# Performance work log

Measured on AMD Instinct MI355X. Metric: run time of the kernel, lower is better.

Reference implementation:

```python
import jax, jax.numpy as jnp
import numpy as np

B, S, DM, H = 4, 1024, 1024, 16
DK = DM // H  # 64, must equal embeddim=64

def _linear(x, W, b):
    # torch nn.Linear: y = x @ W.T + b, W is [out, in]
    return jnp.matmul(x, W.T) + b

def setup_inputs() -> dict:
    key = jax.random.key(0)
    ks = jax.random.split(key, 40)
    inp = {}
    inp["query"] = jax.random.normal(ks[0], (B, S, DM), jnp.float32)
    inp["key"] = jax.random.normal(ks[1], (B, S, DM), jnp.float32)
    inp["value"] = jax.random.normal(ks[2], (B, S, DM), jnp.float32)
    inp["mask"] = jnp.ones((B, S, S), jnp.int32)
    def mk(i, dout, din):
        W = jax.random.normal(ks[i], (dout, din), jnp.float32) / np.sqrt(din).astype(np.float32)
        b = jax.random.normal(ks[i + 20], (dout,), jnp.float32) * 0.01
        return W, b
    # the 4 d_model x d_model projection linears (q, k, v, out)
    inp["Wq"], inp["bq"] = mk(3, DM, DM)
    inp["Wk"], inp["bk"] = mk(4, DM, DM)
    inp["Wv"], inp["bv"] = mk(5, DM, DM)
    inp["Wo"], inp["bo"] = mk(6, DM, DM)
    # the 64x64 refinement linears
    inp["Wkl"], inp["bkl"] = mk(7, DK, DK)   # key_linear
    inp["Wql"], inp["bql"] = mk(8, DK, DK)   # query_linear
    inp["Wq2"], inp["bq2"] = mk(9, DK, DK)   # query2_linear
    inp["Wvl"], inp["bvl"] = mk(10, DK, DK)  # value_linear
    inp["Wel"], inp["bel"] = mk(11, DK, DK)  # embed_linear
    return inp

def reference(query, key, value, mask,
              Wq, bq, Wk, bk, Wv, bv, Wo, bo,
              Wkl, bkl, Wql, bql, Wq2, bq2, Wvl, bvl, Wel, bel):
    b, s, dm = query.shape
    # project and split heads: [b, h, s, d_k]
    def split(x):
        return x.reshape(b, s, H, DK).transpose(0, 2, 1, 3)
    q = split(_linear(query, Wq, bq))
    k = split(_linear(key, Wk, bk))
    v = split(_linear(value, Wv, bv))
    # per-head 64x64 refinements with relu
    key_refine = jax.nn.relu(_linear(k, Wkl, bkl))
    q1 = jax.nn.relu(_linear(q, Wql, bql))
    q1 = jax.nn.relu(_linear(q1, Wel, bel))
    q2 = jax.nn.relu(_linear(q, Wq2, bq2))
    v_refine = jax.nn.relu(_linear(v, Wvl, bvl))
    # two attention-like matmuls (no 1/sqrt(d_k) scaling in original)
    qv = jnp.einsum("bhqd,bhkd->bhqk", q2, v_refine)
    kq = jnp.einsum("bhqd,bhkd->bhqk", q1, key_refine)
    m = mask[:, None, :, :]  # mask.unsqueeze(1)
    kq = jnp.where(m == 0, jnp.float32(-1e9), kq)
    attn = jax.nn.softmax(kq, axis=-1)
    # elementwise combine, then matmul against raw projected key (not value!)
    out = jnp.einsum("bhqk,bhkd->bhqd", attn * qv, k)
    out = out.transpose(0, 2, 1, 3).reshape(b, s, dm)
    return _linear(out, Wo, bo)
```

## Files before the change

kernel.cpp:

```cpp
#include <hip/hip_runtime.h>
#include <hip/hip_bf16.h>

#define B_  4
#define S_  1024
#define DM_ 1024
#define H_  16
#define DK_ 64

typedef unsigned short u16;
typedef __attribute__((ext_vector_type(8))) short bf16x8;
typedef __attribute__((ext_vector_type(4))) float f32x4;

__device__ __forceinline__ float bf2f(u16 u) {
    union { unsigned int i; float f; } c;
    c.i = ((unsigned int)u) << 16;
    return c.f;
}
__device__ __forceinline__ u16 f2bf(float f) {
    union { float f; unsigned int i; } c;
    c.f = f;
    unsigned int x = c.i;
    unsigned int lsb = (x >> 16) & 1u;
    x += 0x7fffu + lsb;
    return (u16)(x >> 16);
}
__device__ __forceinline__ u16 f2bf_fast(float f) {
    __hip_bfloat16 h = __float2bfloat16(f);
    return *reinterpret_cast<u16*>(&h);
}

__device__ __forceinline__ void async_ld16(const u16* g, u16* l) {
    __builtin_amdgcn_global_load_lds(
        (const __attribute__((address_space(1))) unsigned int*)(const void*)g,
        (__attribute__((address_space(3))) unsigned int*)(void*)l, 16, 0, 0);
}

__global__ void detect_kernel(const u16* __restrict__ q, int* __restrict__ flag) {
    int lane = threadIdx.x & 63;
    int cnt = 0;
#pragma unroll
    for (int i = 0; i < 4; ++i) {
        u16 u = q[2 * (lane * 4 + i)];
        int e = (u >> 7) & 0xFF;
        cnt += (e >= 100 && e <= 140) ? 1 : 0;
    }
#pragma unroll
    for (int off = 1; off < 64; off <<= 1) cnt += __shfl_xor(cnt, off, 64);
    if (lane == 0) *flag = (cnt < 128) ? 1 : 0;
}

#define NSEG 12
struct CvtArgs {
    const void* src[NSEG];
    void*       dst[NSEG];
    unsigned    off[NSEG + 1];
};

__global__ __launch_bounds__(256) void prep_kernel(
    CvtArgs a, unsigned total, const int* __restrict__ flag,
    const int* __restrict__ mask, int* __restrict__ tflags)
{
    const int tid = threadIdx.x;
    if (blockIdx.x < 512) {
        const int bx = blockIdx.x;
        const int kt = bx & 15, b = (bx >> 4) & 3, z = bx >> 6;
        int ok = 1;
#pragma unroll
        for (int i = tid; i < 128 * 16; i += 256) {
            int row = z * 128 + (i >> 4), seg = i & 15;
            int4 m = *(const int4*)&mask[((size_t)b * S_ + row) * S_ + kt * 64 + seg * 4];
            ok &= (m.x != 0) & (m.y != 0) & (m.z != 0) & (m.w != 0);
        }
        if (!ok) atomicOr(&tflags[b * 16 + kt], 1);
        return;
    }
    if (!*flag) return;
    unsigned v = (blockIdx.x - 512) * 256 + tid;
    if (v >= total) return;
    int s = 0;
    while (s < NSEG - 1 && v >= a.off[s + 1]) ++s;
    unsigned local = v - a.off[s];
    u16* dp = (u16*)a.dst[s] + (size_t)local * 8;
    const float* sp = (const float*)a.src[s] + (size_t)local * 8;
    float4 x = *(const float4*)sp, y = *(const float4*)(sp + 4);
    u16 t[8] = {f2bf(x.x), f2bf(x.y), f2bf(x.z), f2bf(x.w),
                f2bf(y.x), f2bf(y.y), f2bf(y.z), f2bf(y.w)};
    *(uint4*)dp = *(uint4*)t;
}

struct QKVArgs {
    const u16* A0[3]; const u16* A1[3];
    const u16* W0[3]; const u16* W1[3];
    const void* bias[3];
    const u16* R10[3]; const u16* R11[3];
    const void* rb1[3];
    const u16* R20; const u16* R21; const void* rb2;
    const u16* R30; const u16* R31; const void* rb3;
    u16 *KpT, *q1b, *q2r, *krb, *vrb;
};

__global__ __launch_bounds__(256, 2) void qkv_fused_kernel(
    QKVArgs a, const int* __restrict__ flag)
{
    __shared__ __align__(16) u16 smem[16384];
    u16 (*As)[64] = (u16(*)[64])smem;
    u16 (*Ws)[64] = (u16(*)[64])(smem + 8192);

    const int z = blockIdx.z;
    const int f = *flag;
    const u16* __restrict__ A = f ? a.A1[z] : a.A0[z];
    const u16* __restrict__ W = f ? a.W1[z] : a.W0[z];
    const void* biasp = a.bias[z];

    const int bidf = blockIdx.x;
    const int orig = (bidf & 7) * 32 + (bidf >> 3);
    const int n0   = (orig & 7) * 128;
    const int m0   = (orig >> 3) * 128;

    const int tid  = threadIdx.x;
    const int w    = tid >> 6;
    const int lane = tid & 63;
    const int l16  = lane & 15;
    const int quad = lane >> 4;
    const int wr   = (w >> 1) * 64;
    const int wc   = (w & 1) * 64;

    const int srow = lane >> 3;
    const int sgrp = (lane & 7) ^ srow;

    f32x4 acc[4][4];
#pragma unroll
    for (int rt = 0; rt < 4; ++rt)
#pragma unroll
        for (int ct = 0; ct < 4; ++ct) acc[rt][ct] = (f32x4){0.f, 0.f, 0.f, 0.f};

    for (int k0 = 0; k0 < DM_; k0 += 64) {
#pragma unroll
        for (int s = 0; s < 4; ++s) {
            int seg = w * 4 + s;
            async_ld16(&A[(size_t)(m0 + seg * 8 + srow) * DM_ + k0 + sgrp * 8],
                       &As[seg * 8][0]);
            async_ld16(&W[(size_t)(n0 + seg * 8 + srow) * DM_ + k0 + sgrp * 8],
                       &Ws[seg * 8][0]);
        }
        __syncthreads();
#pragma unroll
        for (int kk = 0; kk < 2; ++kk) {
            const int p = (kk * 4 + quad) ^ (l16 & 7);
            bf16x8 av[4], bv[4];
#pragma unroll
            for (int rt = 0; rt < 4; ++rt)
                av[rt] = *(const bf16x8*)&As[wr + rt * 16 + l16][p * 8];
#pragma unroll
            for (int ct = 0; ct < 4; ++ct)
                bv[ct] = *(const bf16x8*)&Ws[wc + ct * 16 + l16][p * 8];
#pragma unroll
            for (int rt = 0; rt < 4; ++rt)
#pragma unroll
                for (int ct = 0; ct < 4; ++ct)
                    acc[rt][ct] = __builtin_amdgcn_mfma_f32_16x16x32_bf16(
                        av[rt], bv[ct], acc[rt][ct], 0, 0, 0);
        }
        __syncthreads();
    }

    const int hcol = n0 + wc;
    u16 (*Es)[64] = (u16(*)[64])(smem + w * 4096);

#pragma unroll
    for (int ct = 0; ct < 4; ++ct) {
        int col = hcol + ct * 16 + l16;
        float bv = f ? ((const float*)biasp)[col] : bf2f(((const u16*)biasp)[col]);
#pragma unroll
        for (int rt = 0; rt < 4; ++rt) {
            u16 pk[4];
#pragma unroll
            for (int r = 0; r < 4; ++r) {
                int ml = rt * 16 + quad * 4 + r;
                int cl = ct * 16 + l16;
                u16 bb = f2bf(acc[rt][ct][r] + bv);
                pk[r] = bb;
                Es[ml][((((cl >> 3) ^ (ml & 7)) << 3) | (cl & 7))] = bb;
            }
            if (z == 1) {
                int mg = m0 + wr + rt * 16 + quad * 4;
                int b_ = mg >> 10, s_ = mg & 1023;
                int h_ = hcol >> 6, d_ = ct * 16 + l16;
                size_t idx = ((size_t)(b_ * H_ + h_) * DK_ + d_) * S_ + s_;
                *(uint2*)&a.KpT[idx] = *(const uint2*)pk;
            }
        }
    }

    bf16x8 af[4][2];
#pragma unroll
    for (int rt = 0; rt < 4; ++rt)
#pragma unroll
        for (int kk = 0; kk < 2; ++kk)
            af[rt][kk] = *(const bf16x8*)
                &Es[rt * 16 + l16][(((kk * 4 + quad) ^ (l16 & 7)) << 3)];

    const u16* R1 = f ? a.R11[z] : a.R10[z];
    bf16x8 wb[2][4];
#pragma unroll
    for (int kk = 0; kk < 2; ++kk)
#pragma unroll
        for (int ct = 0; ct < 4; ++ct)
            wb[kk][ct] = *(const bf16x8*)
                &R1[(size_t)(ct * 16 + l16) * 64 + kk * 32 + quad * 8];

    f32x4 r1[4][4];
#pragma unroll
    for (int rt = 0; rt < 4; ++rt)
#pragma unroll
        for (int ct = 0; ct < 4; ++ct) r1[rt][ct] = (f32x4){0.f, 0.f, 0.f, 0.f};
#pragma unroll
    for (int kk = 0; kk < 2; ++kk)
#pragma unroll
        for (int rt = 0; rt < 4; ++rt)
#pragma unroll
            for (int ct = 0; ct < 4; ++ct)
                r1[rt][ct] = __builtin_amdgcn_mfma_f32_16x16x32_bf16(
                    af[rt][kk], wb[kk][ct], r1[rt][ct], 0, 0, 0);

    if (z != 0) {
        const void* rb = a.rb1[z];
        u16* out = (z == 1) ? a.krb : a.vrb;
#pragma unroll
        for (int ct = 0; ct < 4; ++ct) {
            int cl = ct * 16 + l16;
            float bv = f ? ((const float*)rb)[cl] : bf2f(((const u16*)rb)[cl]);
#pragma unroll
            for (int rt = 0; rt < 4; ++rt)
#pragma unroll
                for (int r = 0; r < 4; ++r) {
                    float v = r1[rt][ct][r] + bv;
                    v = v > 0.f ? v : 0.f;
                    out[(size_t)(m0 + wr + rt * 16 + quad * 4 + r) * DM_ + hcol + cl]
                        = f2bf(v);
                }
        }
    } else {
        {
            const void* rb = a.rb1[0];
#pragma unroll
            for (int ct = 0; ct < 4; ++ct) {
                int cl = ct * 16 + l16;
                float bv = f ? ((const float*)rb)[cl] : bf2f(((const u16*)rb)[cl]);
#pragma unroll
                for (int rt = 0; rt < 4; ++rt)
#pragma unroll
                    for (int r = 0; r < 4; ++r) {
                        float v = r1[rt][ct][r] + bv;
                        v = v > 0.f ? v : 0.f;
                        int ml = rt * 16 + quad * 4 + r;
                        Es[ml][((((cl >> 3) ^ (ml & 7)) << 3) | (cl & 7))] = f2bf(v);
                    }
            }
        }
        {
            const u16* R3 = f ? a.R31 : a.R30;
#pragma unroll
            for (int kk = 0; kk < 2; ++kk)
#pragma unroll
                for (int ct = 0; ct < 4; ++ct)
                    wb[kk][ct] = *(const bf16x8*)
                        &R3[(size_t)(ct * 16 + l16) * 64 + kk * 32 + quad * 8];
            f32x4 r3[4][4];
#pragma unroll
            for (int rt = 0; rt < 4; ++rt)
#pragma unroll
                for (int ct = 0; ct < 4; ++ct) r3[rt][ct] = (f32x4){0.f, 0.f, 0.f, 0.f};
#pragma unroll
            for (int kk = 0; kk < 2; ++kk)
#pragma unroll
                for (int rt = 0; rt < 4; ++rt)
#pragma unroll
                    for (int ct = 0; ct < 4; ++ct)
                        r3[rt][ct] = __builtin_amdgcn_mfma_f32_16x16x32_bf16(
                            af[rt][kk], wb[kk][ct], r3[rt][ct], 0, 0, 0);
            const void* rb = a.rb3;
#pragma unroll
            for (int ct = 0; ct < 4; ++ct) {
                int cl = ct * 16 + l16;
                float bv = f ? ((const float*)rb)[cl] : bf2f(((const u16*)rb)[cl]);
#pragma unroll
                for (int rt = 0; rt < 4; ++rt)
#pragma unroll
                    for (int r = 0; r < 4; ++r) {
                        float v = r3[rt][ct][r] + bv;
                        v = v > 0.f ? v : 0.f;
                        a.q2r[(size_t)(m0 + wr + rt * 16 + quad * 4 + r) * DM_
                              + hcol + cl] = f2bf(v);
                    }
            }
        }
        {
#pragma unroll
            for (int rt = 0; rt < 4; ++rt)
#pragma unroll
                for (int kk = 0; kk < 2; ++kk)
                    af[rt][kk] = *(const bf16x8*)
                        &Es[rt * 16 + l16][(((kk * 4 + quad) ^ (l16 & 7)) << 3)];
            const u16* R2 = f ? a.R21 : a.R20;
#pragma unroll
            for (int kk = 0; kk < 2; ++kk)
#pragma unroll
                for (int ct = 0; ct < 4; ++ct)
                    wb[kk][ct] = *(const bf16x8*)
                        &R2[(size_t)(ct * 16 + l16) * 64 + kk * 32 + quad * 8];
            f32x4 r2[4][4];
#pragma unroll
            for (int rt = 0; rt < 4; ++rt)
#pragma unroll
                for (int ct = 0; ct < 4; ++ct) r2[rt][ct] = (f32x4){0.f, 0.f, 0.f, 0.f};
#pragma unroll
            for (int kk = 0; kk < 2; ++kk)
#pragma unroll
                for (int rt = 0; rt < 4; ++rt)
#pragma unroll
                    for (int ct = 0; ct < 4; ++ct)
                        r2[rt][ct] = __builtin_amdgcn_mfma_f32_16x16x32_bf16(
                            af[rt][kk], wb[kk][ct], r2[rt][ct], 0, 0, 0);
            const void* rb = a.rb2;
#pragma unroll
            for (int ct = 0; ct < 4; ++ct) {
                int cl = ct * 16 + l16;
                float bv = f ? ((const float*)rb)[cl] : bf2f(((const u16*)rb)[cl]);
#pragma unroll
                for (int rt = 0; rt < 4; ++rt)
#pragma unroll
                    for (int r = 0; r < 4; ++r) {
                        float v = r2[rt][ct][r] + bv;
                        v = v > 0.f ? v : 0.f;
                        a.q1b[(size_t)(m0 + wr + rt * 16 + quad * 4 + r) * DM_
                              + hcol + cl] = f2bf(v);
                    }
            }
        }
    }
}

__global__ __launch_bounds__(256, 2) void gemm_async_kernel(
    const u16* __restrict__ Ain, const u16* __restrict__ W0,
    const u16* __restrict__ W1, const void* __restrict__ biasp,
    void* __restrict__ Cp, const int* __restrict__ flag)
{
    __shared__ __align__(16) u16 As[128][64];
    __shared__ __align__(16) u16 Ws[128][64];

    const int f = *flag;
    const u16* __restrict__ W = f ? W1 : W0;

    const int bidf = blockIdx.x;
    const int orig = (bidf & 7) * 32 + (bidf >> 3);
    const int n0   = (orig & 7) * 128;
    const int m0   = (orig >> 3) * 128;

    const int tid  = threadIdx.x;
    const int w    = tid >> 6;
    const int lane = tid & 63;
    const int l16  = lane & 15;
    const int quad = lane >> 4;
    const int wr   = (w >> 1) * 64;
    const int wc   = (w & 1) * 64;

    const int srow = lane >> 3;
    const int sgrp = (lane & 7) ^ srow;

    f32x4 acc[4][4];
#pragma unroll
    for (int rt = 0; rt < 4; ++rt)
#pragma unroll
        for (int ct = 0; ct < 4; ++ct) acc[rt][ct] = (f32x4){0.f, 0.f, 0.f, 0.f};

    for (int k0 = 0; k0 < DM_; k0 += 64) {
#pragma unroll
        for (int s = 0; s < 4; ++s) {
            int seg = w * 4 + s;
            async_ld16(&Ain[(size_t)(m0 + seg * 8 + srow) * DM_ + k0 + sgrp * 8],
                       &As[seg * 8][0]);
            async_ld16(&W[(size_t)(n0 + seg * 8 + srow) * DM_ + k0 + sgrp * 8],
                       &Ws[seg * 8][0]);
        }
        __syncthreads();
#pragma unroll
        for (int kk = 0; kk < 2; ++kk) {
            const int p = (kk * 4 + quad) ^ (l16 & 7);
            bf16x8 av[4], bv[4];
#pragma unroll
            for (int rt = 0; rt < 4; ++rt)
                av[rt] = *(const bf16x8*)&As[wr + rt * 16 + l16][p * 8];
#pragma unroll
            for (int ct = 0; ct < 4; ++ct)
                bv[ct] = *(const bf16x8*)&Ws[wc + ct * 16 + l16][p * 8];
#pragma unroll
            for (int rt = 0; rt < 4; ++rt)
#pragma unroll
                for (int ct = 0; ct < 4; ++ct)
                    acc[rt][ct] = __builtin_amdgcn_mfma_f32_16x16x32_bf16(
                        av[rt], bv[ct], acc[rt][ct], 0, 0, 0);
        }
        __syncthreads();
    }

#pragma unroll
    for (int ct = 0; ct < 4; ++ct) {
        int col = n0 + wc + ct * 16 + l16;
        float bv = f ? ((const float*)biasp)[col] : bf2f(((const u16*)biasp)[col]);
#pragma unroll
        for (int rt = 0; rt < 4; ++rt)
#pragma unroll
            for (int r = 0; r < 4; ++r) {
                int row = m0 + wr + rt * 16 + quad * 4 + r;
                float v = acc[rt][ct][r] + bv;
                size_t idx = (size_t)row * DM_ + col;
                if (f) ((float*)Cp)[idx] = v;
                else   ((u16*)Cp)[idx]   = f2bf(v);
            }
    }
}

__global__ __launch_bounds__(256, 2) void attn_kernel(
    const u16* __restrict__ q1, const u16* __restrict__ q2,
    const u16* __restrict__ kr, const u16* __restrict__ vr,
    const u16* __restrict__ kpt, const int* __restrict__ mask,
    const int* __restrict__ tflags, u16* __restrict__ om)
{
    __shared__ __align__(16) u16 krs[2][64][64];
    __shared__ __align__(16) u16 vrs[2][64][64];
    __shared__ __align__(16) u16 kts[2][64][64];

    const int bid  = blockIdx.x;
    const int orig = (bid & 7) * 64 + (bid >> 3);
    const int qt = orig & 7;
    const int h  = (orig >> 3) & 15;
    const int b  = orig >> 7;

    const int q0   = qt * 128;
    const int tid  = threadIdx.x;
    const int w    = tid >> 6;
    const int lane = tid & 63;
    const int l16  = lane & 15;
    const int quad = lane >> 4;

    const size_t base  = (size_t)b * S_ * DM_ + (size_t)h * DK_;
    const size_t baseT = (size_t)(b * H_ + h) * DK_ * S_;

    const int srow = lane >> 3;
    const int sgrp = (lane & 7) ^ srow;

#define STAGE_TILES(buf, kn)                                                   \
    {                                                                          \
        _Pragma("unroll")                                                      \
        for (int i = 0; i < 6; ++i) {                                          \
            int s_ = w * 6 + i;                                                \
            int t_ = s_ >> 3;                                                  \
            int r8 = (s_ & 7) * 8;                                             \
            if (t_ == 0)                                                       \
                async_ld16(&kr[base + (size_t)((kn) + r8 + srow) * DM_ +       \
                               sgrp * 8], &krs[buf][r8][0]);                   \
            else if (t_ == 1)                                                  \
                async_ld16(&vr[base + (size_t)((kn) + r8 + srow) * DM_ +       \
                               sgrp * 8], &vrs[buf][r8][0]);                   \
            else                                                               \
                async_ld16(&kpt[baseT + (size_t)(r8 + srow) * S_ + (kn) +      \
                                sgrp * 8], &kts[buf][r8][0]);                  \
        }                                                                      \
    }

    bf16x8 a1[2][2], a2[2][2];
#pragma unroll
    for (int rt = 0; rt < 2; ++rt) {
        const int qrow = q0 + w * 32 + rt * 16 + l16;
#pragma unroll
        for (int kk = 0; kk < 2; ++kk) {
            a1[rt][kk] = *(const bf16x8*)&q1[base + (size_t)qrow * DM_ + kk * 32 + quad * 8];
            a2[rt][kk] = *(const bf16x8*)&q2[base + (size_t)qrow * DM_ + kk * 32 + quad * 8];
        }
    }

    float m_run[2], l_run[2];
    f32x4 oacc[2][4];
#pragma unroll
    for (int qt2 = 0; qt2 < 2; ++qt2) { m_run[qt2] = -1e30f; l_run[qt2] = 0.f; }
#pragma unroll
    for (int rt = 0; rt < 2; ++rt)
#pragma unroll
        for (int ct = 0; ct < 4; ++ct) oacc[rt][ct] = (f32x4){0.f, 0.f, 0.f, 0.f};

    STAGE_TILES(0, 0)
    __syncthreads();

    for (int kt = 0; kt < S_ / 64; ++kt) {
        const int cur = kt & 1;
        const int k0  = kt * 64;
        const bool pf = (kt + 1 < S_ / 64);

        if (pf) STAGE_TILES(cur ^ 1, k0 + 64)

        const int tf = tflags[b * 16 + kt];

        f32x4 st1[2][4], st2[2][4];
#pragma unroll
        for (int qt2 = 0; qt2 < 2; ++qt2)
#pragma unroll
            for (int kt4 = 0; kt4 < 4; ++kt4) {
                st1[qt2][kt4] = (f32x4){0.f, 0.f, 0.f, 0.f};
                st2[qt2][kt4] = (f32x4){0.f, 0.f, 0.f, 0.f};
            }
        __builtin_amdgcn_s_setprio(1);
#pragma unroll
        for (int kk = 0; kk < 2; ++kk) {
            const int p = ((kk * 4 + quad) ^ (l16 & 7)) * 8;
            bf16x8 b1[4], b2[4];
#pragma unroll
            for (int kt4 = 0; kt4 < 4; ++kt4) {
                b1[kt4] = *(const bf16x8*)&krs[cur][kt4 * 16 + l16][p];
                b2[kt4] = *(const bf16x8*)&vrs[cur][kt4 * 16 + l16][p];
            }
#pragma unroll
            for (int qt2 = 0; qt2 < 2; ++qt2)
#pragma unroll
                for (int kt4 = 0; kt4 < 4; ++kt4) {
                    st1[qt2][kt4] = __builtin_amdgcn_mfma_f32_16x16x32_bf16(
                        b1[kt4], a1[qt2][kk], st1[qt2][kt4], 0, 0, 0);
                    st2[qt2][kt4] = __builtin_amdgcn_mfma_f32_16x16x32_bf16(
                        b2[kt4], a2[qt2][kk], st2[qt2][kt4], 0, 0, 0);
                }
        }
        __builtin_amdgcn_s_setprio(0);

        if (tf) {
#pragma unroll
            for (int qt2 = 0; qt2 < 2; ++qt2)
#pragma unroll
                for (int kt4 = 0; kt4 < 4; ++kt4)
#pragma unroll
                    for (int r = 0; r < 4; ++r) {
                        int qrow = q0 + w * 32 + qt2 * 16 + l16;
                        int kc   = k0 + kt4 * 16 + quad * 4 + r;
                        if (mask[((size_t)b * S_ + qrow) * S_ + kc] == 0)
                            st1[qt2][kt4][r] = -1e9f;
                    }
        }

        float alphaq[2], newm[2];
#pragma unroll
        for (int qt2 = 0; qt2 < 2; ++qt2) {
            float m = st1[qt2][0][0];
#pragma unroll
            for (int kt4 = 0; kt4 < 4; ++kt4)
#pragma unroll
                for (int r = 0; r < 4; ++r)
                    m = fmaxf(m, st1[qt2][kt4][r]);
            m = fmaxf(m, __shfl_xor(m, 16, 64));
            m = fmaxf(m, __shfl_xor(m, 32, 64));
            newm[qt2]   = fmaxf(m_run[qt2], m);
            alphaq[qt2] = __expf(m_run[qt2] - newm[qt2]);
            m_run[qt2]  = newm[qt2];
        }

        unsigned pk[2][4][2];
#pragma unroll
        for (int qt2 = 0; qt2 < 2; ++qt2) {
            float s = 0.f;
#pragma unroll
            for (int kt4 = 0; kt4 < 4; ++kt4)
#pragma unroll
                for (int pp = 0; pp < 2; ++pp) {
                    float p0 = __expf(st1[qt2][kt4][2 * pp]     - newm[qt2]);
                    float p1 = __expf(st1[qt2][kt4][2 * pp + 1] - newm[qt2]);
                    s += p0 + p1;
                    pk[qt2][kt4][pp] =
                        (unsigned)f2bf_fast(p0 * st2[qt2][kt4][2 * pp])
                        | ((unsigned)f2bf_fast(p1 * st2[qt2][kt4][2 * pp + 1]) << 16);
                }
            s += __shfl_xor(s, 16, 64);
            s += __shfl_xor(s, 32, 64);
            l_run[qt2] = l_run[qt2] * alphaq[qt2] + s;
        }

#pragma unroll
        for (int rt = 0; rt < 2; ++rt)
#pragma unroll
            for (int r = 0; r < 4; ++r) {
                float ao = __shfl(alphaq[rt], quad * 4 + r, 64);
#pragma unroll
                for (int ct = 0; ct < 4; ++ct) oacc[rt][ct][r] *= ao;
            }

        {
            __builtin_amdgcn_s_setprio(1);
            bf16x8 bb[2][4];
#pragma unroll
            for (int kk = 0; kk < 2; ++kk) {
                const int p = ((kk * 4 + quad) ^ (l16 & 7)) * 8;
#pragma unroll
                for (int ct = 0; ct < 4; ++ct)
                    bb[kk][ct] = *(const bf16x8*)&kts[cur][ct * 16 + l16][p];
            }
#pragma unroll
            for (int rt = 0; rt < 2; ++rt)
#pragma unroll
                for (int kk = 0; kk < 2; ++kk) {
                    union { unsigned u[4]; bf16x8 v; } pa;
#pragma unroll
                    for (int j = 0; j < 4; ++j) {
                        int src = (2 * (quad & 1) + (j >> 1)) * 16 + l16;
                        unsigned lo = __shfl(pk[rt][2 * kk][j & 1],     src, 64);
                        unsigned hi = __shfl(pk[rt][2 * kk + 1][j & 1], src, 64);
                        pa.u[j] = (quad >> 1) ? hi : lo;
                    }
#pragma unroll
                    for (int ct = 0; ct < 4; ++ct)
                        oacc[rt][ct] = __builtin_amdgcn_mfma_f32_16x16x32_bf16(
                            pa.v, bb[kk][ct], oacc[rt][ct], 0, 0, 0);
                }
            __builtin_amdgcn_s_setprio(0);
        }

        if (pf) __syncthreads();
    }

#pragma unroll
    for (int rt = 0; rt < 2; ++rt)
#pragma unroll
        for (int r = 0; r < 4; ++r) {
            float lo = __shfl(l_run[rt], quad * 4 + r, 64);
            float inv = 1.f / lo;
#pragma unroll
            for (int ct = 0; ct < 4; ++ct) {
                int row = q0 + w * 32 + rt * 16 + quad * 4 + r;
                int col = ct * 16 + l16;
                om[base + (size_t)row * DM_ + col] = f2bf_fast(oacc[rt][ct][r] * inv);
            }
        }
#undef STAGE_TILES
}

extern "C" void kernel_launch(void* const* d_in, const int* in_sizes, int n_in,
                              void* d_out, int out_size, void* d_ws, size_t ws_size,
                              hipStream_t stream)
{
    const void* query = d_in[0];
    const void* key   = d_in[1];
    const void* value = d_in[2];
    const int*  mask  = (const int*)d_in[3];
    const void* Wq  = d_in[4];  const void* bq  = d_in[5];
    const void* Wk  = d_in[6];  const void* bk  = d_in[7];
    const void* Wv  = d_in[8];  const void* bv  = d_in[9];
    const void* Wo  = d_in[10]; const void* bo  = d_in[11];
    const void* Wkl = d_in[12]; const void* bkl = d_in[13];
    const void* Wql = d_in[14]; const void* bql = d_in[15];
    const void* Wq2 = d_in[16]; const void* bq2 = d_in[17];
    const void* Wvl = d_in[18]; const void* bvl = d_in[19];
    const void* Wel = d_in[20]; const void* bel = d_in[21];

    int* flag   = (int*)d_ws;
    int* tflags = (int*)d_ws + 4;
    u16* ws     = (u16*)((char*)d_ws + 512);
    const size_t BUF = (size_t)(B_ * S_) * DM_;
    u16* Kp  = ws + 0 * BUF;
    u16* krb = ws + 1 * BUF;
    u16* q1b = ws + 2 * BUF;
    u16* q2r = ws + 3 * BUF;
    u16* vrb = ws + 4 * BUF;
    u16* Om  = ws + 5 * BUF;
    u16* KpT = ws + 6 * BUF;
    u16* Qc  = ws + 7 * BUF;
    u16* Kc  = ws + 8 * BUF;
    u16* Vc  = ws + 9 * BUF;
    u16* Wbig = ws + 10 * BUF;
    u16* Wqc = Wbig + 0 * (size_t)(DM_ * DM_);
    u16* Wkc = Wbig + 1 * (size_t)(DM_ * DM_);
    u16* Wvc = Wbig + 2 * (size_t)(DM_ * DM_);
    u16* Woc = Wbig + 3 * (size_t)(DM_ * DM_);
    u16* Wsm = Wbig + 4 * (size_t)(DM_ * DM_);
    u16* Wklc = Wsm + 0 * (DK_ * DK_);
    u16* Wqlc = Wsm + 1 * (DK_ * DK_);
    u16* Welc = Wsm + 2 * (DK_ * DK_);
    u16* Wq2c = Wsm + 3 * (DK_ * DK_);
    u16* Wvlc = Wsm + 4 * (DK_ * DK_);
    (void)Kp;

    const int M = B_ * S_;
    dim3 blk(256);

    detect_kernel<<<1, 64, 0, stream>>>((const u16*)query, flag);

    hipMemsetAsync(tflags, 0, 64 * sizeof(int), stream);
    CvtArgs ca;
    const unsigned VIN = (unsigned)(BUF / 8);
    const unsigned VWB = (unsigned)(DM_ * DM_ / 8);
    const unsigned VWS = (unsigned)(DK_ * DK_ / 8);
    const void* srcs[NSEG] = {query, key, value, Wq, Wk, Wv, Wo, Wkl, Wql, Wel, Wq2, Wvl};
    void* dsts[NSEG] = {Qc, Kc, Vc, Wqc, Wkc, Wvc, Woc, Wklc, Wqlc, Welc, Wq2c, Wvlc};
    unsigned vcn[NSEG] = {VIN, VIN, VIN, VWB, VWB, VWB, VWB, VWS, VWS, VWS, VWS, VWS};
    unsigned off = 0;
    for (int i = 0; i < NSEG; ++i) { ca.src[i] = srcs[i]; ca.dst[i] = dsts[i]; ca.off[i] = off; off += vcn[i]; }
    ca.off[NSEG] = off;
    prep_kernel<<<dim3(512 + (off + 255) / 256), blk, 0, stream>>>(ca, off, flag, mask, tflags);

    QKVArgs qa = {};
    qa.A0[0] = (const u16*)query; qa.A1[0] = Qc;
    qa.A0[1] = (const u16*)key;   qa.A1[1] = Kc;
    qa.A0[2] = (const u16*)value; qa.A1[2] = Vc;
    qa.W0[0] = (const u16*)Wq; qa.W1[0] = Wqc;
    qa.W0[1] = (const u16*)Wk; qa.W1[1] = Wkc;
    qa.W0[2] = (const u16*)Wv; qa.W1[2] = Wvc;
    qa.bias[0] = bq; qa.bias[1] = bk; qa.bias[2] = bv;
    qa.R10[0] = (const u16*)Wql; qa.R11[0] = Wqlc; qa.rb1[0] = bql;
    qa.R10[1] = (const u16*)Wkl; qa.R11[1] = Wklc; qa.rb1[1] = bkl;
    qa.R10[2] = (const u16*)Wvl; qa.R11[2] = Wvlc; qa.rb1[2] = bvl;
    qa.R20 = (const u16*)Wel; qa.R21 = Welc; qa.rb2 = bel;
    qa.R30 = (const u16*)Wq2; qa.R31 = Wq2c; qa.rb3 = bq2;
    qa.KpT = KpT; qa.q1b = q1b; qa.q2r = q2r; qa.krb = krb; qa.vrb = vrb;
    dim3 gBig(256, 1, 3);
    qkv_fused_kernel<<<gBig, blk, 0, stream>>>(qa, flag);

    attn_kernel<<<dim3(512), blk, 0, stream>>>(q1b, q2r, krb, vrb, KpT, mask, tflags, Om);

    gemm_async_kernel<<<dim3(256), blk, 0, stream>>>(Om, (const u16*)Wo, Woc, bo, d_out, flag);
}
```

Measured before the change: 274.4 us.

## Double-buffer LDS tiles in QKV and output projection GEMMs

Both the fused QKV projection kernel and the generic GEMM kernel switch from a single LDS tile to two ping-pong buffers. The next K-slice is prefetched asynchronously into the alternate buffer while MFMAs run on the current one, and one of the two barriers per iteration is removed. The goal is to hide global-to-LDS load latency behind the matrix math. In exchange, LDS use per block doubles to 64KB, which could limit occupancy. The barrier still waits on all outstanding loads, so only part of the load latency is hidden.

```diff
diff --git a/kernel.cpp b/kernel.cpp
--- a/kernel.cpp
+++ b/kernel.cpp
@@ -102,9 +102,8 @@
 __global__ __launch_bounds__(256, 2) void qkv_fused_kernel(
     QKVArgs a, const int* __restrict__ flag)
 {
-    __shared__ __align__(16) u16 smem[16384];
-    u16 (*As)[64] = (u16(*)[64])smem;
-    u16 (*Ws)[64] = (u16(*)[64])(smem + 8192);
+    __shared__ __align__(16) u16 As2[2][128][64];
+    __shared__ __align__(16) u16 Ws2[2][128][64];
 
     const int z = blockIdx.z;
     const int f = *flag;
@@ -128,32 +127,41 @@
     const int srow = lane >> 3;
     const int sgrp = (lane & 7) ^ srow;
 
+#define QSTAGE(buf, kq)                                                        \
+    {                                                                          \
+        _Pragma("unroll")                                                      \
+        for (int s = 0; s < 4; ++s) {                                          \
+            int seg = w * 4 + s;                                               \
+            async_ld16(&A[(size_t)(m0 + seg * 8 + srow) * DM_ + (kq) +         \
+                          sgrp * 8], &As2[buf][seg * 8][0]);                   \
+            async_ld16(&W[(size_t)(n0 + seg * 8 + srow) * DM_ + (kq) +         \
+                          sgrp * 8], &Ws2[buf][seg * 8][0]);                   \
+        }                                                                      \
+    }
+
     f32x4 acc[4][4];
 #pragma unroll
     for (int rt = 0; rt < 4; ++rt)
 #pragma unroll
         for (int ct = 0; ct < 4; ++ct) acc[rt][ct] = (f32x4){0.f, 0.f, 0.f, 0.f};
 
+    QSTAGE(0, 0)
+    __syncthreads();
+
     for (int k0 = 0; k0 < DM_; k0 += 64) {
-#pragma unroll
-        for (int s = 0; s < 4; ++s) {
-            int seg = w * 4 + s;
-            async_ld16(&A[(size_t)(m0 + seg * 8 + srow) * DM_ + k0 + sgrp * 8],
-                       &As[seg * 8][0]);
-            async_ld16(&W[(size_t)(n0 + seg * 8 + srow) * DM_ + k0 + sgrp * 8],
-                       &Ws[seg * 8][0]);
-        }
-        __syncthreads();
+        const int cur = (k0 >> 6) & 1;
+        const bool pf = (k0 + 64 < DM_);
+        if (pf) QSTAGE(cur ^ 1, k0 + 64)
 #pragma unroll
         for (int kk = 0; kk < 2; ++kk) {
             const int p = (kk * 4 + quad) ^ (l16 & 7);
             bf16x8 av[4], bv[4];
 #pragma unroll
             for (int rt = 0; rt < 4; ++rt)
-                av[rt] = *(const bf16x8*)&As[wr + rt * 16 + l16][p * 8];
+                av[rt] = *(const bf16x8*)&As2[cur][wr + rt * 16 + l16][p * 8];
 #pragma unroll
             for (int ct = 0; ct < 4; ++ct)
-                bv[ct] = *(const bf16x8*)&Ws[wc + ct * 16 + l16][p * 8];
+                bv[ct] = *(const bf16x8*)&Ws2[cur][wc + ct * 16 + l16][p * 8];
 #pragma unroll
             for (int rt = 0; rt < 4; ++rt)
 #pragma unroll
@@ -161,11 +169,12 @@
                     acc[rt][ct] = __builtin_amdgcn_mfma_f32_16x16x32_bf16(
                         av[rt], bv[ct], acc[rt][ct], 0, 0, 0);
         }
-        __syncthreads();
-    }
+        if (pf) __syncthreads();
+    }
+    __syncthreads();
 
     const int hcol = n0 + wc;
-    u16 (*Es)[64] = (u16(*)[64])(smem + w * 4096);
+    u16 (*Es)[64] = (u16(*)[64])((u16*)As2 + w * 4096);
 
 #pragma unroll
     for (int ct = 0; ct < 4; ++ct) {
@@ -339,6 +348,7 @@
             }
         }
     }
+#undef QSTAGE
 }
 
 __global__ __launch_bounds__(256, 2) void gemm_async_kernel(
@@ -346,8 +356,8 @@
     const u16* __restrict__ W1, const void* __restrict__ biasp,
     void* __restrict__ Cp, const int* __restrict__ flag)
 {
-    __shared__ __align__(16) u16 As[128][64];
-    __shared__ __align__(16) u16 Ws[128][64];
+    __shared__ __align__(16) u16 As2[2][128][64];
+    __shared__ __align__(16) u16 Ws2[2][128][64];
 
     const int f = *flag;
     const u16* __restrict__ W = f ? W1 : W0;
@@ -368,32 +378,41 @@
     const int srow = lane >> 3;
     const int sgrp = (lane & 7) ^ srow;
 
+#define GSTAGE(buf, kq)                                                        \
+    {                                                                          \
+        _Pragma("unroll")                                                      \
+        for (int s = 0; s < 4; ++s) {                                          \
+            int seg = w * 4 + s;                                               \
+            async_ld16(&Ain[(size_t)(m0 + seg * 8 + srow) * DM_ + (kq) +       \
+                            sgrp * 8], &As2[buf][seg * 8][0]);                 \
+            async_ld16(&W[(size_t)(n0 + seg * 8 + srow) * DM_ + (kq) +         \
+                          sgrp * 8], &Ws2[buf][seg * 8][0]);                   \
+        }                                                                      \
+    }
+
     f32x4 acc[4][4];
 #pragma unroll
     for (int rt = 0; rt < 4; ++rt)
 #pragma unroll
         for (int ct = 0; ct < 4; ++ct) acc[rt][ct] = (f32x4){0.f, 0.f, 0.f, 0.f};
 
+    GSTAGE(0, 0)
+    __syncthreads();
+
     for (int k0 = 0; k0 < DM_; k0 += 64) {
-#pragma unroll
-        for (int s = 0; s < 4; ++s) {
-            int seg = w * 4 + s;
-            async_ld16(&Ain[(size_t)(m0 + seg * 8 + srow) * DM_ + k0 + sgrp * 8],
-                       &As[seg * 8][0]);
-            async_ld16(&W[(size_t)(n0 + seg * 8 + srow) * DM_ + k0 + sgrp * 8],
-                       &Ws[seg * 8][0]);
-        }
-        __syncthreads();
+        const int cur = (k0 >> 6) & 1;
+        const bool pf = (k0 + 64 < DM_);
+        if (pf) GSTAGE(cur ^ 1, k0 + 64)
 #pragma unroll
         for (int kk = 0; kk < 2; ++kk) {
             const int p = (kk * 4 + quad) ^ (l16 & 7);
             bf16x8 av[4], bv[4];
 #pragma unroll
             for (int rt = 0; rt < 4; ++rt)
-                av[rt] = *(const bf16x8*)&As[wr + rt * 16 + l16][p * 8];
+                av[rt] = *(const bf16x8*)&As2[cur][wr + rt * 16 + l16][p * 8];
 #pragma unroll
             for (int ct = 0; ct < 4; ++ct)
-                bv[ct] = *(const bf16x8*)&Ws[wc + ct * 16 + l16][p * 8];
+                bv[ct] = *(const bf16x8*)&Ws2[cur][wc + ct * 16 + l16][p * 8];
 #pragma unroll
             for (int rt = 0; rt < 4; ++rt)
 #pragma unroll
@@ -401,7 +420,7 @@
                     acc[rt][ct] = __builtin_amdgcn_mfma_f32_16x16x32_bf16(
                         av[rt], bv[ct], acc[rt][ct], 0, 0, 0);
         }
-        __syncthreads();
+        if (pf) __syncthreads();
     }
 
 #pragma unroll
@@ -419,6 +438,7 @@
                 else   ((u16*)Cp)[idx]   = f2bf(v);
             }
     }
+#undef GSTAGE
 }
 
 __global__ __launch_bounds__(256, 2) void attn_kernel(
```

Result: slower. 283.8 us (+3.4%).
